# Kernel tuning notes

Measured on AMD Instinct MI355X. Metric: run time of the kernel, lower is better.

The kernel has to match this reference:

```python
import jax, jax.numpy as jnp
import numpy as np

B, S, H, D = 512, 77, 12, 64
E = H * D  # 768


def setup_inputs() -> dict:
    key = jax.random.key(0)
    ks = jax.random.split(key, 9)
    std = 1.0 / np.sqrt(E)
    x = jax.random.normal(ks[0], (B, S, E), dtype=jnp.float32)
    wq = jax.random.uniform(ks[1], (E, E), jnp.float32, -std, std)
    bq = jax.random.uniform(ks[2], (E,), jnp.float32, -std, std)
    wk = jax.random.uniform(ks[3], (E, E), jnp.float32, -std, std)
    bk = jax.random.uniform(ks[4], (E,), jnp.float32, -std, std)
    wv = jax.random.uniform(ks[5], (E, E), jnp.float32, -std, std)
    bv = jax.random.uniform(ks[6], (E,), jnp.float32, -std, std)
    wo = jax.random.uniform(ks[7], (E, E), jnp.float32, -std, std)
    bo = jax.random.uniform(ks[8], (E,), jnp.float32, -std, std)
    return {"x": x, "wq": wq, "bq": bq, "wk": wk, "bk": bk,
            "wv": wv, "bv": bv, "wo": wo, "bo": bo}


def reference(x, wq, bq, wk, bk, wv, bv, wo, bo):
    b = x.shape[0]
    scale = 0.125  # 1/sqrt(64)
    q = (x @ wq + bq) * scale          # [b, S, E]
    k = x @ wk + bk
    v = x @ wv + bv
    # split heads: [b, H, S, D]
    q = q.reshape(b, S, H, D).transpose(0, 2, 1, 3)
    k = k.reshape(b, S, H, D).transpose(0, 2, 1, 3)
    v = v.reshape(b, S, H, D).transpose(0, 2, 1, 3)
    scores = jnp.einsum("bhsd,bhtd->bhst", q, k)  # [b, H, S, S]
    # causal mask: strictly-upper = -inf, else 0 (matches triu_(1) on -inf fill)
    mask = jnp.triu(jnp.full((S, S), -jnp.inf, dtype=scores.dtype), k=1)
    attn = jax.nn.softmax(scores + mask, axis=-1)
    out = jnp.einsum("bhst,bhtd->bhsd", attn, v)  # [b, H, S, D]
    out = out.transpose(0, 2, 1, 3).reshape(b, S, E)
    return out @ wo + bo
```

## Files before the change

kernel.cpp:

```cpp
#include <hip/hip_runtime.h>

#define S_LEN 77
#define NHEAD 12
#define DHEAD 64
#define EMB   768
#define BATCH 512
#define MROWS (BATCH * S_LEN)
#define NQKV  (3 * EMB)
#define KDIM  768
#define NKT   (KDIM / 64)

typedef __attribute__((ext_vector_type(8))) short bf16x8;
typedef __attribute__((ext_vector_type(4))) float f32x4;

#define WAITV(n) asm volatile("s_waitcnt vmcnt(" #n ")" ::: "memory")
#define WAITL(n) asm volatile("s_waitcnt lgkmcnt(" #n ")" ::: "memory")

__device__ __forceinline__ unsigned short f2bf(float f) {
  union { float f; unsigned int u; } v; v.f = f;
  unsigned int r = (v.u + 0x7fffu + ((v.u >> 16) & 1u)) >> 16;
  return (unsigned short)r;
}

__device__ __forceinline__ void gload_lds16(const void* g, void* l) {
  __builtin_amdgcn_global_load_lds((__attribute__((address_space(1))) void*)g,
                                   (__attribute__((address_space(3))) void*)l,
                                   16, 0, 0);
}

__global__ void cvt_f32_bf16(const float4* __restrict__ in,
                             ushort4* __restrict__ out, int n4) {
  int stride = gridDim.x * blockDim.x;
  for (int i = blockIdx.x * blockDim.x + threadIdx.x; i < n4; i += stride) {
    float4 v = in[i];
    ushort4 o;
    o.x = f2bf(v.x); o.y = f2bf(v.y); o.z = f2bf(v.z); o.w = f2bf(v.w);
    out[i] = o;
  }
}

__global__ void prep_weights(const float* __restrict__ wq, const float* __restrict__ wk,
                             const float* __restrict__ wv, const float* __restrict__ wo,
                             const float* __restrict__ bq, const float* __restrict__ bk,
                             const float* __restrict__ bv,
                             unsigned short* __restrict__ wqkvT,
                             unsigned short* __restrict__ woT,
                             float* __restrict__ bqkv) {
  const int i0 = blockIdx.x * blockDim.x + threadIdx.x;
  const int stride = gridDim.x * blockDim.x;
  const int KB = EMB / 8;
  for (int idx = i0; idx < NQKV * KB; idx += stride) {
    int n = idx / KB, k0 = (idx - n * KB) * 8;
    const float* w; int c;
    if (n < EMB)          { w = wq; c = n; }
    else if (n < 2 * EMB) { w = wk; c = n - EMB; }
    else                  { w = wv; c = n - 2 * EMB; }
    bf16x8 o;
#pragma unroll
    for (int i = 0; i < 8; ++i) o[i] = (short)f2bf(w[(size_t)(k0 + i) * EMB + c]);
    *(bf16x8*)(wqkvT + (size_t)n * EMB + k0) = o;
  }
  for (int idx = i0; idx < EMB * KB; idx += stride) {
    int n = idx / KB, k0 = (idx - n * KB) * 8;
    bf16x8 o;
#pragma unroll
    for (int i = 0; i < 8; ++i) o[i] = (short)f2bf(wo[(size_t)(k0 + i) * EMB + n]);
    *(bf16x8*)(woT + (size_t)n * EMB + k0) = o;
  }
  for (int idx = i0; idx < NQKV; idx += stride) {
    bqkv[idx] = (idx < EMB) ? bq[idx]
              : (idx < 2 * EMB ? bk[idx - EMB] : bv[idx - 2 * EMB]);
  }
}

template <int MODE>
__global__ __launch_bounds__(512, 2) void gemm256(const unsigned short* __restrict__ A,
                                                  const unsigned short* __restrict__ BT,
                                                  const float* __restrict__ bias,
                                                  void* __restrict__ Cout) {
  __shared__ unsigned short lds[2 * 32768];

  const int tid  = threadIdx.x;
  const int wave = tid >> 6;
  const int lane = tid & 63;
  const int wr = wave >> 2;
  const int wc = wave & 3;
  const int fr = lane & 15;
  const int fg = lane >> 4;

  const int ncol = gridDim.x;
  const int nwg  = gridDim.x * gridDim.y;
  const int orig = blockIdx.y * gridDim.x + blockIdx.x;
  const int q8   = nwg >> 3, r8 = nwg & 7;
  const int xcd  = orig & 7, off = orig >> 3;
  const int swz  = (xcd < r8 ? xcd * (q8 + 1) : r8 * (q8 + 1) + (xcd - r8) * q8) + off;
  const int brow = (swz / ncol) * 256;
  const int bcol = (swz % ncol) * 256;

  f32x4 acc[8][4] = {};

  const int grow = (wave >> 2) * 128 + (wave & 3) * 8 + (lane >> 3);
  const int srcc = (lane & 7) ^ ((lane >> 3) & 7);
  const unsigned short* gA = A  + (size_t)(brow + grow) * KDIM + srcc * 8;
  const unsigned short* gB = BT + (size_t)(bcol + grow) * KDIM + srcc * 8;
  const int wbase = (wave >> 2) * 8192 + (wave & 3) * 512;

  auto ALOAD = [&](int t, int j) {
    gload_lds16(gA + (size_t)(j * 32) * KDIM + t * 64,
                lds + (t & 1) * 32768 + wbase + j * 2048);
  };
  auto BLOAD = [&](int t, int j) {
    gload_lds16(gB + (size_t)(j * 32) * KDIM + t * 64,
                lds + (t & 1) * 32768 + 16384 + wbase + j * 2048);
  };

  const int rsw = fr & 7;

  #pragma unroll
  for (int j = 0; j < 4; ++j) BLOAD(0, j);
  #pragma unroll
  for (int j = 0; j < 4; ++j) ALOAD(0, j);
  WAITV(2);
  __builtin_amdgcn_sched_barrier(0);
  __builtin_amdgcn_s_barrier();

  for (int t = 0; t < NKT; ++t) {
    const bool st = (t + 1 < NKT);
    const unsigned short* sb  = lds + (t & 1) * 32768;
    const unsigned short* sbB = sb + 16384;
    bf16x8 bfr[4][2];
    #pragma unroll
    for (int p = 0; p < 4; ++p) {
      if (p == 0) {
        #pragma unroll
        for (int n = 0; n < 4; ++n)
          #pragma unroll
          for (int kk = 0; kk < 2; ++kk)
            bfr[n][kk] = *(const bf16x8*)(sbB + (wc * 64 + n * 16 + fr) * 64 +
                                          (((kk * 4 + fg) ^ rsw) * 8));
      }
      bf16x8 afr[2][2];
      #pragma unroll
      for (int mi = 0; mi < 2; ++mi)
        #pragma unroll
        for (int kk = 0; kk < 2; ++kk)
          afr[mi][kk] = *(const bf16x8*)(sb + (wr * 128 + (2 * p + mi) * 16 + fr) * 64 +
                                         (((kk * 4 + fg) ^ rsw) * 8));
      if (st) {
        if (p < 2) { BLOAD(t + 1, 2 * p);     BLOAD(t + 1, 2 * p + 1); }
        else       { ALOAD(t + 1, 2 * p - 4); ALOAD(t + 1, 2 * p - 3); }
      }
      __builtin_amdgcn_sched_barrier(0);
      __builtin_amdgcn_s_barrier();
      asm volatile("s_waitcnt lgkmcnt(0)" ::: "memory");
      __builtin_amdgcn_sched_barrier(0);
      __builtin_amdgcn_s_setprio(1);
      #pragma unroll
      for (int kk = 0; kk < 2; ++kk)
        #pragma unroll
        for (int mi = 0; mi < 2; ++mi)
          #pragma unroll
          for (int n = 0; n < 4; ++n)
            acc[2 * p + mi][n] = __builtin_amdgcn_mfma_f32_16x16x32_bf16(
                afr[mi][kk], bfr[n][kk], acc[2 * p + mi][n], 0, 0, 0);
      __builtin_amdgcn_s_setprio(0);
      __builtin_amdgcn_sched_barrier(0);
      if (p == 1) { if (st) { WAITV(4); } else { WAITV(0); } }
      if (p == 3 && st) { WAITV(2); }
      __builtin_amdgcn_s_barrier();
    }
  }

  float bvals[4];
#pragma unroll
  for (int n = 0; n < 4; ++n) bvals[n] = bias[bcol + wc * 64 + n * 16 + fr];
#pragma unroll
  for (int m = 0; m < 8; ++m) {
#pragma unroll
    for (int r = 0; r < 4; ++r) {
      const int row = brow + wr * 128 + m * 16 + fg * 4 + r;
#pragma unroll
      for (int n = 0; n < 4; ++n) {
        const int col = bcol + wc * 64 + n * 16 + fr;
        float v = acc[m][n][r] + bvals[n];
        if (MODE == 0) {
          if (col < EMB) v *= 0.125f;
          ((unsigned short*)Cout)[(size_t)row * NQKV + col] = f2bf(v);
        } else {
          ((float*)Cout)[(size_t)row * EMB + col] = v;
        }
      }
    }
  }
}

#define SV 104
__global__ __launch_bounds__(320) void attn_kernel(const unsigned short* __restrict__ qkv,
                                                   unsigned short* __restrict__ attn_out) {
  __shared__ unsigned short vT_lds[64 * SV];
  __shared__ unsigned short p_lds[80 * SV];

  const int tid  = threadIdx.x;
  const int wv_  = tid >> 6;
  const int lane = tid & 63;
  const int fr = lane & 15;
  const int fg = lane >> 4;

  const int bh = blockIdx.x;
  const int b  = bh / NHEAD;
  const int h  = bh - b * NHEAD;

  const size_t base = (size_t)b * S_LEN * NQKV + (size_t)h * DHEAD;

  bf16x8 qfr[2], kfr[5][2];
  {
    const int srow = wv_ * 16 + fr;
    const int qs = (srow < S_LEN) ? srow : 0;
    const unsigned short* qg = qkv + base + (size_t)qs * NQKV + fg * 8;
    qfr[0] = *(const bf16x8*)(qg);
    qfr[1] = *(const bf16x8*)(qg + 32);
    const unsigned short* kg = qkv + base + EMB + fg * 8;
#pragma unroll
    for (int n = 0; n < 5; ++n)
#pragma unroll
      for (int kk = 0; kk < 2; ++kk)
        kfr[n][kk] = *(const bf16x8*)(kg + (size_t)(n * 16 + fr) * NQKV + kk * 32);
  }

  for (int i = tid; i < 64 * 19; i += 320) {
    int d = i / 19, c = 77 + (i - d * 19);
    vT_lds[d * SV + c] = 0;
  }
  for (int i = tid; i < 80 * 16; i += 320) {
    int s = i >> 4, c = 80 + (i & 15);
    p_lds[s * SV + c] = 0;
  }

  for (int idx = tid; idx < S_LEN * 32; idx += 320) {
    int s = idx >> 5, c = idx & 31;
    unsigned int vx = *(const unsigned int*)(qkv + base + (size_t)s * NQKV + 2 * EMB + c * 2);
    vT_lds[(c * 2 + 0) * SV + s] = (unsigned short)(vx & 0xffffu);
    vT_lds[(c * 2 + 1) * SV + s] = (unsigned short)(vx >> 16);
  }

  f32x4 sc[5];
#pragma unroll
  for (int n = 0; n < 5; ++n) sc[n] = (f32x4){0.f, 0.f, 0.f, 0.f};
#pragma unroll
  for (int kk = 0; kk < 2; ++kk)
#pragma unroll
    for (int n = 0; n < 5; ++n)
      sc[n] = __builtin_amdgcn_mfma_f32_16x16x32_bf16(qfr[kk], kfr[n][kk], sc[n], 0, 0, 0);

  float mrow[4], ssum[4];
#pragma unroll
  for (int r = 0; r < 4; ++r) {
    const int s_loc = wv_ * 16 + fg * 4 + r;
    float mx = -1e30f;
#pragma unroll
    for (int n = 0; n < 5; ++n) {
      const int t = n * 16 + fr;
      float val = ((t <= s_loc) && (t < S_LEN)) ? sc[n][r] : -1e30f;
      sc[n][r] = val;
      mx = fmaxf(mx, val);
    }
    mrow[r] = mx;
  }
#pragma unroll
  for (int off = 1; off < 16; off <<= 1)
#pragma unroll
    for (int r = 0; r < 4; ++r)
      mrow[r] = fmaxf(mrow[r], __shfl_xor(mrow[r], off, 64));
#pragma unroll
  for (int r = 0; r < 4; ++r) {
    float sm = 0.f;
#pragma unroll
    for (int n = 0; n < 5; ++n) {
      float p = __expf(sc[n][r] - mrow[r]);
      sc[n][r] = p;
      sm += p;
    }
    ssum[r] = sm;
  }
#pragma unroll
  for (int off = 1; off < 16; off <<= 1)
#pragma unroll
    for (int r = 0; r < 4; ++r)
      ssum[r] += __shfl_xor(ssum[r], off, 64);

#pragma unroll
  for (int r = 0; r < 4; ++r) {
    const int srow = wv_ * 16 + fg * 4 + r;
    const float inv = 1.0f / ssum[r];
#pragma unroll
    for (int n = 0; n < 5; ++n)
      p_lds[srow * SV + n * 16 + fr] = f2bf(sc[n][r] * inv);
  }
  __syncthreads();

  f32x4 o[4];
#pragma unroll
  for (int n = 0; n < 4; ++n) o[n] = (f32x4){0.f, 0.f, 0.f, 0.f};
#pragma unroll
  for (int kk = 0; kk < 96; kk += 32) {
    bf16x8 afr = *(const bf16x8*)(p_lds + (wv_ * 16 + fr) * SV + kk + fg * 8);
#pragma unroll
    for (int n = 0; n < 4; ++n) {
      bf16x8 bfr = *(const bf16x8*)(vT_lds + (n * 16 + fr) * SV + kk + fg * 8);
      o[n] = __builtin_amdgcn_mfma_f32_16x16x32_bf16(afr, bfr, o[n], 0, 0, 0);
    }
  }

  const size_t obase = (size_t)b * S_LEN * EMB + (size_t)h * DHEAD;
#pragma unroll
  for (int r = 0; r < 4; ++r) {
    const int srow = wv_ * 16 + fg * 4 + r;
    if (srow < S_LEN) {
#pragma unroll
      for (int n = 0; n < 4; ++n)
        attn_out[obase + (size_t)srow * EMB + n * 16 + fr] = f2bf(o[n][r]);
    }
  }
}

extern "C" void kernel_launch(void* const* d_in, const int* in_sizes, int n_in,
                              void* d_out, int out_size, void* d_ws, size_t ws_size,
                              hipStream_t stream) {
  const float* x  = (const float*)d_in[0];
  const float* wq = (const float*)d_in[1];
  const float* bq = (const float*)d_in[2];
  const float* wk = (const float*)d_in[3];
  const float* bk = (const float*)d_in[4];
  const float* wv = (const float*)d_in[5];
  const float* bv = (const float*)d_in[6];
  const float* wo = (const float*)d_in[7];
  const float* bo = (const float*)d_in[8];
  (void)in_sizes; (void)n_in; (void)out_size; (void)ws_size;

  char* ws = (char*)d_ws;
  unsigned short* x_bf   = (unsigned short*)(ws);
  unsigned short* wqkvT  = (unsigned short*)(ws + 60555264ULL);
  unsigned short* woT    = (unsigned short*)(ws + 64094208ULL);
  float*          bqkv   = (float*)         (ws + 65273856ULL);
  unsigned short* qkv    = (unsigned short*)(ws + 65283072ULL);
  unsigned short* attn_o = (unsigned short*)(ws + 246948864ULL);

  cvt_f32_bf16<<<2048, 256, 0, stream>>>((const float4*)x, (ushort4*)x_bf, MROWS * EMB / 4);
  prep_weights<<<1024, 256, 0, stream>>>(wq, wk, wv, wo, bq, bk, bv, wqkvT, woT, bqkv);
  gemm256<0><<<dim3(NQKV / 256, MROWS / 256), 512, 0, stream>>>(x_bf, wqkvT, bqkv, qkv);
  attn_kernel<<<BATCH * NHEAD, 320, 0, stream>>>(qkv, attn_o);
  gemm256<1><<<dim3(EMB / 256, MROWS / 256), 512, 0, stream>>>(attn_o, woT, bo, d_out);
}
```

Measured before the change: 361.6 us.

## Fuse fp32-to-bf16 conversion of x into QKV GEMM A-tile loading

Removes the separate cvt_f32_bf16 pass over x and instead has the QKV GEMM load fp32 A tiles into registers, convert them to bf16, and write them to LDS, with a reworked prefetch and wait schedule for MODE 0. This drops a full read and write of the bf16 copy of x. In exchange the GEMM reads twice the bytes for A, needs extra registers for the staged tile, and replaces the async global-to-LDS path with a register round trip, which may reduce overlap. Because x columns are each read three times (once per N-tile group), the fp32 traffic is repeated as well.

Result: slower. 414.3 us (+14.6%).

```diff
diff --git a/kernel.cpp b/kernel.cpp
--- a/kernel.cpp
+++ b/kernel.cpp
@@ -15,6 +15,7 @@
 
 #define WAITV(n) asm volatile("s_waitcnt vmcnt(" #n ")" ::: "memory")
 #define WAITL(n) asm volatile("s_waitcnt lgkmcnt(" #n ")" ::: "memory")
+#define SB()     __builtin_amdgcn_sched_barrier(0)
 
 __device__ __forceinline__ unsigned short f2bf(float f) {
   union { float f; unsigned int u; } v; v.f = f;
@@ -26,17 +27,6 @@
   __builtin_amdgcn_global_load_lds((__attribute__((address_space(1))) void*)g,
                                    (__attribute__((address_space(3))) void*)l,
                                    16, 0, 0);
-}
-
-__global__ void cvt_f32_bf16(const float4* __restrict__ in,
-                             ushort4* __restrict__ out, int n4) {
-  int stride = gridDim.x * blockDim.x;
-  for (int i = blockIdx.x * blockDim.x + threadIdx.x; i < n4; i += stride) {
-    float4 v = in[i];
-    ushort4 o;
-    o.x = f2bf(v.x); o.y = f2bf(v.y); o.z = f2bf(v.z); o.w = f2bf(v.w);
-    out[i] = o;
-  }
 }
 
 __global__ void prep_weights(const float* __restrict__ wq, const float* __restrict__ wk,
@@ -75,6 +65,7 @@
 
 template <int MODE>
 __global__ __launch_bounds__(512, 2) void gemm256(const unsigned short* __restrict__ A,
+                                                  const float* __restrict__ Af,
                                                   const unsigned short* __restrict__ BT,
                                                   const float* __restrict__ bias,
                                                   void* __restrict__ Cout) {
@@ -101,7 +92,8 @@
 
   const int grow = (wave >> 2) * 128 + (wave & 3) * 8 + (lane >> 3);
   const int srcc = (lane & 7) ^ ((lane >> 3) & 7);
-  const unsigned short* gA = A  + (size_t)(brow + grow) * KDIM + srcc * 8;
+  const unsigned short* gA = (MODE == 1) ? A + (size_t)(brow + grow) * KDIM + srcc * 8 : nullptr;
+  const float*          gF = (MODE == 0) ? Af + (size_t)(brow + grow) * KDIM + srcc * 8 : nullptr;
   const unsigned short* gB = BT + (size_t)(bcol + grow) * KDIM + srcc * 8;
   const int wbase = (wave >> 2) * 8192 + (wave & 3) * 512;
 
@@ -114,14 +106,45 @@
                 lds + (t & 1) * 32768 + 16384 + wbase + j * 2048);
   };
 
+  f32x4 areg[8];
+#define AGLB(t)                                                                 \
+  { _Pragma("unroll")                                                           \
+    for (int j = 0; j < 4; ++j) {                                               \
+      const float* p = gF + (size_t)(j * 32) * KDIM + (t) * 64;                 \
+      areg[2 * j]     = *(const f32x4*)(p);                                     \
+      areg[2 * j + 1] = *(const f32x4*)(p + 4);                                 \
+    } }
+#define AWRITE(t)                                                               \
+  { _Pragma("unroll")                                                           \
+    for (int j = 0; j < 4; ++j) {                                               \
+      bf16x8 o;                                                                 \
+      _Pragma("unroll")                                                         \
+      for (int i = 0; i < 4; ++i) o[i]     = (short)f2bf(areg[2 * j][i]);       \
+      _Pragma("unroll")                                                         \
+      for (int i = 0; i < 4; ++i) o[4 + i] = (short)f2bf(areg[2 * j + 1][i]);   \
+      *(bf16x8*)(lds + ((t) & 1) * 32768 + wbase + j * 2048 + lane * 8) = o;    \
+    } }
+
   const int rsw = fr & 7;
 
-  #pragma unroll
-  for (int j = 0; j < 4; ++j) BLOAD(0, j);
-  #pragma unroll
-  for (int j = 0; j < 4; ++j) ALOAD(0, j);
-  WAITV(2);
-  __builtin_amdgcn_sched_barrier(0);
+  if (MODE == 0) {
+    AGLB(0);
+    SB();
+    #pragma unroll
+    for (int j = 0; j < 4; ++j) BLOAD(0, j);
+    WAITV(4); SB();
+    AWRITE(0);
+    WAITL(0);
+    WAITV(0);
+    SB();
+  } else {
+    #pragma unroll
+    for (int j = 0; j < 4; ++j) BLOAD(0, j);
+    #pragma unroll
+    for (int j = 0; j < 4; ++j) ALOAD(0, j);
+    WAITV(2);
+    SB();
+  }
   __builtin_amdgcn_s_barrier();
 
   for (int t = 0; t < NKT; ++t) {
@@ -146,14 +169,26 @@
         for (int kk = 0; kk < 2; ++kk)
           afr[mi][kk] = *(const bf16x8*)(sb + (wr * 128 + (2 * p + mi) * 16 + fr) * 64 +
                                          (((kk * 4 + fg) ^ rsw) * 8));
-      if (st) {
-        if (p < 2) { BLOAD(t + 1, 2 * p);     BLOAD(t + 1, 2 * p + 1); }
-        else       { ALOAD(t + 1, 2 * p - 4); ALOAD(t + 1, 2 * p - 3); }
+      if (MODE == 0) {
+        if (p == 0 && st) {
+          AGLB(t + 1);
+          SB();
+          BLOAD(t + 1, 0); BLOAD(t + 1, 1); BLOAD(t + 1, 2); BLOAD(t + 1, 3);
+        }
+        if (p == 2 && st) {
+          WAITV(4); SB();
+          AWRITE(t + 1);
+        }
+      } else {
+        if (st) {
+          if (p < 2) { BLOAD(t + 1, 2 * p);     BLOAD(t + 1, 2 * p + 1); }
+          else       { ALOAD(t + 1, 2 * p - 4); ALOAD(t + 1, 2 * p - 3); }
+        }
       }
-      __builtin_amdgcn_sched_barrier(0);
+      SB();
       __builtin_amdgcn_s_barrier();
       asm volatile("s_waitcnt lgkmcnt(0)" ::: "memory");
-      __builtin_amdgcn_sched_barrier(0);
+      SB();
       __builtin_amdgcn_s_setprio(1);
       #pragma unroll
       for (int kk = 0; kk < 2; ++kk)
@@ -164,12 +199,19 @@
             acc[2 * p + mi][n] = __builtin_amdgcn_mfma_f32_16x16x32_bf16(
                 afr[mi][kk], bfr[n][kk], acc[2 * p + mi][n], 0, 0, 0);
       __builtin_amdgcn_s_setprio(0);
-      __builtin_amdgcn_sched_barrier(0);
-      if (p == 1) { if (st) { WAITV(4); } else { WAITV(0); } }
-      if (p == 3 && st) { WAITV(2); }
+      SB();
+      if (MODE == 0) {
+        if (p == 3 && st) { WAITV(0); }
+        if (p == 1 && !st) { WAITV(0); }
+      } else {
+        if (p == 1) { if (st) { WAITV(4); } else { WAITV(0); } }
+        if (p == 3 && st) { WAITV(2); }
+      }
       __builtin_amdgcn_s_barrier();
     }
   }
+#undef AGLB
+#undef AWRITE
 
   float bvals[4];
 #pragma unroll
@@ -338,16 +380,14 @@
   (void)in_sizes; (void)n_in; (void)out_size; (void)ws_size;
 
   char* ws = (char*)d_ws;
-  unsigned short* x_bf   = (unsigned short*)(ws);
   unsigned short* wqkvT  = (unsigned short*)(ws + 60555264ULL);
   unsigned short* woT    = (unsigned short*)(ws + 64094208ULL);
   float*          bqkv   = (float*)         (ws + 65273856ULL);
   unsigned short* qkv    = (unsigned short*)(ws + 65283072ULL);
   unsigned short* attn_o = (unsigned short*)(ws + 246948864ULL);
 
-  cvt_f32_bf16<<<2048, 256, 0, stream>>>((const float4*)x, (ushort4*)x_bf, MROWS * EMB / 4);
   prep_weights<<<1024, 256, 0, stream>>>(wq, wk, wv, wo, bq, bk, bv, wqkvT, woT, bqkv);
-  gemm256<0><<<dim3(NQKV / 256, MROWS / 256), 512, 0, stream>>>(x_bf, wqkvT, bqkv, qkv);
+  gemm256<0><<<dim3(NQKV / 256, MROWS / 256), 512, 0, stream>>>(nullptr, x, wqkvT, bqkv, qkv);
   attn_kernel<<<BATCH * NHEAD, 320, 0, stream>>>(qkv, attn_o);
-  gemm256<1><<<dim3(EMB / 256, MROWS / 256), 512, 0, stream>>>(attn_o, woT, bo, d_out);
-}
+  gemm256<1><<<dim3(EMB / 256, MROWS / 256), 512, 0, stream>>>(attn_o, nullptr, woT, bo, d_out);
+}
```
